# Kernel tuning notes

Measured on AMD Instinct MI355X. Metric: run time of the kernel, lower is better.

The kernel has to match this reference:

```python
import jax, jax.numpy as jnp
import numpy as np

N_LAYERS = 5
HID = 64
N_FF = 512
N_VOCAB = 500
N_NODES = 50000
N_EDGES = 800000


def setup_inputs() -> dict:
    key = jax.random.key(0)
    ks = jax.random.split(key, 12)
    x = jax.random.randint(ks[0], (N_NODES,), 0, N_VOCAB)
    edge_index = jax.random.randint(ks[1], (2, N_EDGES), 0, N_NODES)
    edge_attr = jax.random.normal(ks[2], (N_EDGES, 4), dtype=jnp.float32)
    s = 1.0 / float(np.sqrt(HID))
    vert_emb = jax.random.normal(ks[3], (N_VOCAB + 1, HID), dtype=jnp.float32) * s
    vert_emb = vert_emb.at[N_VOCAB].set(0.0)  # padding_idx row
    edge_emb_w = jax.random.normal(ks[4], (4, HID), dtype=jnp.float32) * 0.5
    edge_lin_w = jax.random.normal(ks[5], (N_LAYERS, HID, HID), dtype=jnp.float32) * s
    rel_w = jax.random.normal(ks[6], (N_LAYERS, HID, HID), dtype=jnp.float32) * s
    rel_b = jnp.zeros((N_LAYERS, HID), dtype=jnp.float32)
    root_w = jax.random.normal(ks[7], (N_LAYERS, HID, HID), dtype=jnp.float32) * s
    res_w = jax.random.normal(ks[8], (N_LAYERS, HID, HID), dtype=jnp.float32) * s
    head_w1 = jax.random.normal(ks[9], (HID, N_FF), dtype=jnp.float32) * s
    head_b1 = jnp.zeros((N_FF,), dtype=jnp.float32)
    head_w2 = jax.random.normal(ks[10], (N_FF, 1), dtype=jnp.float32) * (1.0 / float(np.sqrt(N_FF)))
    head_b2 = jnp.zeros((1,), dtype=jnp.float32)
    return dict(x=x, edge_index=edge_index, edge_attr=edge_attr, vert_emb=vert_emb,
                edge_emb_w=edge_emb_w, edge_lin_w=edge_lin_w, rel_w=rel_w, rel_b=rel_b,
                root_w=root_w, res_w=res_w, head_w1=head_w1, head_b1=head_b1,
                head_w2=head_w2, head_b2=head_b2)


def reference(x, edge_index, edge_attr, vert_emb, edge_emb_w, edge_lin_w, rel_w, rel_b,
              root_w, res_w, head_w1, head_b1, head_w2, head_b2):
    src, dst = edge_index[0], edge_index[1]
    h = vert_emb[x]                         # [N, HID] embedding lookup
    ea = edge_attr @ edge_emb_w             # [E, HID] edge embedding
    n = h.shape[0]
    for l in range(N_LAYERS):
        ea_l = ea @ edge_lin_w[l]           # ResGraphModule.edge_lin
        # GraphConv(aggr='add'): lin_rel(scatter_add(x_src * e)) + lin_root(x)
        msg = h[src] * ea_l                 # [E, HID] gather + modulate
        agg = jax.ops.segment_sum(msg, dst, num_segments=n)
        out = agg @ rel_w[l] + rel_b[l] + h @ root_w[l]
        out = jax.nn.relu(out)
        h = out + h @ res_w[l]              # residual branch (res_lin)
    # head MLP (dropout is identity in eval mode); torch GELU is exact erf GELU
    hft = jax.nn.gelu(h @ head_w1 + head_b1, approximate=False)
    return hft @ head_w2 + head_b2          # [N, 1]
```

## Files before the change

kernel.cpp:

```cpp
#include <hip/hip_runtime.h>
#include <math.h>

#define HID 64
#define NLAY 5
#define NFF 512

typedef __attribute__((ext_vector_type(8))) short bf16x8;
typedef __attribute__((ext_vector_type(4))) float f32x4;

__device__ __forceinline__ unsigned short f2bf(float x) {
  unsigned int b = __float_as_uint(x);
  b += 0x7FFFu + ((b >> 16) & 1u);
  return (unsigned short)(b >> 16);
}
__device__ __forceinline__ float bf2f(unsigned short u) {
  return __uint_as_float((unsigned int)u << 16);
}

__global__ void prep_wl_kernel(const float* __restrict__ edge_emb_w,
                               const float* __restrict__ edge_lin_w,
                               float* __restrict__ Wl) {
  int l = blockIdx.x;
  int t = threadIdx.x;
  int j = t >> 6;
  int d = t & 63;
  const float* ew = edge_emb_w + j * HID;
  const float* lw = edge_lin_w + l * HID * HID;
  float acc = 0.f;
#pragma unroll
  for (int k = 0; k < HID; ++k) acc = fmaf(ew[k], lw[k * HID + d], acc);
  Wl[(l * 4 + j) * HID + d] = acc;
}

__global__ void prep_w1b_kernel(const float* __restrict__ w1,
                                unsigned short* __restrict__ w1bhi,
                                unsigned short* __restrict__ w1blo) {
  int t = blockIdx.x * 256 + threadIdx.x;
  int f = t >> 6;
  int l = t & 63;
  int kt = f >> 5;
  int nt = f & 31;
  int krow = kt * 32 + (l >> 4) * 8;
  int col = nt * 16 + (l & 15);
#pragma unroll
  for (int j = 0; j < 8; ++j) {
    float v = w1[(size_t)(krow + j) * NFF + col];
    unsigned short hi = f2bf(v);
    unsigned short lo = f2bf(v - bf2f(hi));
    w1bhi[(size_t)t * 8 + j] = hi;
    w1blo[(size_t)t * 8 + j] = lo;
  }
}

__global__ void prep_nw_kernel(const float* __restrict__ rel_w,
                               const float* __restrict__ root_w,
                               const float* __restrict__ res_w,
                               unsigned short* __restrict__ nwhi,
                               unsigned short* __restrict__ nwlo) {
  int mi = blockIdx.x;
  int layer = mi / 3, mat = mi % 3;
  const float* W = (mat == 0 ? rel_w : (mat == 1 ? root_w : res_w)) +
                   (size_t)layer * HID * HID;
  int t = threadIdx.x;
  int f = t >> 6, l = t & 63;
  int kt = f >> 2, nt = f & 3;
  int krow = kt * 32 + (l >> 4) * 8;
  int col = nt * 16 + (l & 15);
#pragma unroll
  for (int j = 0; j < 8; ++j) {
    float v = W[(size_t)(krow + j) * HID + col];
    unsigned short hi = f2bf(v);
    unsigned short lo = f2bf(v - bf2f(hi));
    size_t off = (((size_t)mi * 8 + f) * 64 + l) * 8 + j;
    nwhi[off] = hi;
    nwlo[off] = lo;
  }
}

__global__ void embed_kernel(const int* __restrict__ x,
                             const float* __restrict__ vert_emb,
                             float* __restrict__ h,
                             unsigned short* __restrict__ h16, int n) {
  int idx = blockIdx.x * blockDim.x + threadIdx.x;
  if (idx >= n * HID) return;
  int node = idx >> 6;
  int d = idx & 63;
  float v = vert_emb[x[node] * HID + d];
  h[idx] = v;
  h16[idx] = f2bf(v);
}


__global__ void zero_deg_kernel(int* __restrict__ deg, int n) {
  int i = blockIdx.x * blockDim.x + threadIdx.x;
  if (i < n) deg[i] = 0;
}

__global__ void hist_kernel(const int* __restrict__ dst, int* __restrict__ deg, int E) {
  int e = blockIdx.x * blockDim.x + threadIdx.x;
  if (e < E) atomicAdd(&deg[dst[e]], 1);
}

__global__ void bsum_kernel(const int* __restrict__ deg, int* __restrict__ bsum, int n) {
  __shared__ int s[256];
  int t = threadIdx.x;
  int i = blockIdx.x * 256 + t;
  s[t] = (i < n) ? deg[i] : 0;
  __syncthreads();
#pragma unroll
  for (int off = 128; off > 0; off >>= 1) {
    if (t < off) s[t] += s[t + off];
    __syncthreads();
  }
  if (t == 0) bsum[blockIdx.x] = s[0];
}

__global__ void bscan_kernel(const int* __restrict__ bsum, int* __restrict__ boff, int nb) {
  __shared__ int s[256];
  int t = threadIdx.x;
  int v = (t < nb) ? bsum[t] : 0;
  s[t] = v;
  __syncthreads();
#pragma unroll
  for (int off = 1; off < 256; off <<= 1) {
    int u = (t >= off) ? s[t - off] : 0;
    __syncthreads();
    s[t] += u;
    __syncthreads();
  }
  if (t < nb) boff[t] = s[t] - v;
}

__global__ void scan3_kernel(const int* __restrict__ deg, const int* __restrict__ boff,
                             int* __restrict__ row_ptr, int* __restrict__ cursor, int n) {
  __shared__ int s[256];
  int t = threadIdx.x;
  int i = blockIdx.x * 256 + t;
  int v = (i < n) ? deg[i] : 0;
  s[t] = v;
  __syncthreads();
#pragma unroll
  for (int off = 1; off < 256; off <<= 1) {
    int u = (t >= off) ? s[t - off] : 0;
    __syncthreads();
    s[t] += u;
    __syncthreads();
  }
  if (i < n) {
    int excl = boff[blockIdx.x] + s[t] - v;
    row_ptr[i] = excl;
    cursor[i] = excl;
    if (i == n - 1) row_ptr[n] = excl + v;
  }
}

__global__ void scatter_kernel(const int* __restrict__ src,
                               const int* __restrict__ dst,
                               const float4* __restrict__ edge_attr,
                               int* __restrict__ cursor,
                               float4* __restrict__ csr2, int E) {
  int e = blockIdx.x * blockDim.x + threadIdx.x;
  if (e >= E) return;
  int pos = atomicAdd(&cursor[dst[e]], 1);
  csr2[(size_t)2 * pos] = edge_attr[e];
  float4 m;
  m.x = __int_as_float(src[e]);
  m.y = 0.f; m.z = 0.f; m.w = 0.f;
  csr2[(size_t)2 * pos + 1] = m;
}

__global__ __launch_bounds__(256, 8)
void gather_kernel(const int* __restrict__ row_ptr,
                   const float4* __restrict__ csr2,
                   const float* __restrict__ Wl,
                   const unsigned short* __restrict__ h16,
                   float* __restrict__ agg, int n) {
  int wid = threadIdx.x >> 6;
  int d = threadIdx.x & 63;
  int node = blockIdx.x * 4 + wid;
  if (node >= n) return;
  int beg = __builtin_amdgcn_readfirstlane(row_ptr[node]);
  int end = __builtin_amdgcn_readfirstlane(row_ptr[node + 1]);
  const int* csri = (const int*)csr2;
  float P0 = 0.f, P1 = 0.f, P2 = 0.f, P3 = 0.f;
  int j = beg;
  for (; j + 16 <= end; j += 16) {
    int ss[16];
    float hh[16];
    float4 ee[16];
#pragma unroll
    for (int u = 0; u < 16; ++u) ss[u] = csri[((size_t)2 * (j + u) + 1) * 4];
#pragma unroll
    for (int u = 0; u < 16; ++u) hh[u] = bf2f(h16[(size_t)ss[u] * HID + d]);
#pragma unroll
    for (int u = 0; u < 16; ++u) ee[u] = csr2[(size_t)2 * (j + u)];
#pragma unroll
    for (int u = 0; u < 16; ++u) {
      P0 = fmaf(ee[u].x, hh[u], P0);
      P1 = fmaf(ee[u].y, hh[u], P1);
      P2 = fmaf(ee[u].z, hh[u], P2);
      P3 = fmaf(ee[u].w, hh[u], P3);
    }
  }
  for (; j + 4 <= end; j += 4) {
    int ss[4];
    float hh[4];
    float4 ee[4];
#pragma unroll
    for (int u = 0; u < 4; ++u) ss[u] = csri[((size_t)2 * (j + u) + 1) * 4];
#pragma unroll
    for (int u = 0; u < 4; ++u) hh[u] = bf2f(h16[(size_t)ss[u] * HID + d]);
#pragma unroll
    for (int u = 0; u < 4; ++u) ee[u] = csr2[(size_t)2 * (j + u)];
#pragma unroll
    for (int u = 0; u < 4; ++u) {
      P0 = fmaf(ee[u].x, hh[u], P0);
      P1 = fmaf(ee[u].y, hh[u], P1);
      P2 = fmaf(ee[u].z, hh[u], P2);
      P3 = fmaf(ee[u].w, hh[u], P3);
    }
  }
  for (; j < end; ++j) {
    int s0 = csri[((size_t)2 * j + 1) * 4];
    float4 e0 = csr2[(size_t)2 * j];
    float h0 = bf2f(h16[(size_t)s0 * HID + d]);
    P0 = fmaf(e0.x, h0, P0);
    P1 = fmaf(e0.y, h0, P1);
    P2 = fmaf(e0.z, h0, P2);
    P3 = fmaf(e0.w, h0, P3);
  }
  float acc = P0 * Wl[d];
  acc = fmaf(P1, Wl[HID + d], acc);
  acc = fmaf(P2, Wl[2 * HID + d], acc);
  acc = fmaf(P3, Wl[3 * HID + d], acc);
  agg[(size_t)node * HID + d] = acc;
}

__global__ __launch_bounds__(256, 4)
void node_mfma_kernel(const float* __restrict__ h,
                      const unsigned short* __restrict__ h16,
                      const float* __restrict__ agg,
                      const unsigned short* __restrict__ nwhi,
                      const unsigned short* __restrict__ nwlo,
                      const float* __restrict__ rel_b,
                      float* __restrict__ hn,
                      unsigned short* __restrict__ hn16, int n) {
  int tid = threadIdx.x;
  int w = tid >> 6;
  int l = tid & 63;
  int q = l & 15;
  int g = l >> 4;
  int base = blockIdx.x * 16;
  int node = base + q;
  if (node >= n) node = n - 1;
  bf16x8 aghi[2], aglo[2], ahhi[2], ahlo[2];
#pragma unroll
  for (int kt = 0; kt < 2; ++kt) {
    int koff = kt * 32 + g * 8;
    const float* ap = agg + (size_t)node * HID + koff;
    const float* hp = h + (size_t)node * HID + koff;
    ahhi[kt] = *(const bf16x8*)(h16 + (size_t)node * HID + koff);
#pragma unroll
    for (int j = 0; j < 8; ++j) {
      float av = ap[j];
      unsigned short hi = f2bf(av);
      aghi[kt][j] = (short)hi;
      aglo[kt][j] = (short)f2bf(av - bf2f(hi));
      float r = hp[j] - bf2f((unsigned short)ahhi[kt][j]);
      ahlo[kt][j] = (short)f2bf(r);
    }
  }
  f32x4 aR = {0.f, 0.f, 0.f, 0.f};
  f32x4 aO = {0.f, 0.f, 0.f, 0.f};
  f32x4 aS = {0.f, 0.f, 0.f, 0.f};
#pragma unroll
  for (int kt = 0; kt < 2; ++kt) {
    int f = kt * 4 + w;
    const bf16x8* bRh = (const bf16x8*)(nwhi + (((size_t)0 * 8 + f) * 64 + l) * 8);
    const bf16x8* bRl = (const bf16x8*)(nwlo + (((size_t)0 * 8 + f) * 64 + l) * 8);
    const bf16x8* bOh = (const bf16x8*)(nwhi + (((size_t)1 * 8 + f) * 64 + l) * 8);
    const bf16x8* bOl = (const bf16x8*)(nwlo + (((size_t)1 * 8 + f) * 64 + l) * 8);
    const bf16x8* bSh = (const bf16x8*)(nwhi + (((size_t)2 * 8 + f) * 64 + l) * 8);
    const bf16x8* bSl = (const bf16x8*)(nwlo + (((size_t)2 * 8 + f) * 64 + l) * 8);
    aR = __builtin_amdgcn_mfma_f32_16x16x32_bf16(aglo[kt], *bRh, aR, 0, 0, 0);
    aR = __builtin_amdgcn_mfma_f32_16x16x32_bf16(aghi[kt], *bRl, aR, 0, 0, 0);
    aR = __builtin_amdgcn_mfma_f32_16x16x32_bf16(aghi[kt], *bRh, aR, 0, 0, 0);
    aO = __builtin_amdgcn_mfma_f32_16x16x32_bf16(ahlo[kt], *bOh, aO, 0, 0, 0);
    aO = __builtin_amdgcn_mfma_f32_16x16x32_bf16(ahhi[kt], *bOl, aO, 0, 0, 0);
    aO = __builtin_amdgcn_mfma_f32_16x16x32_bf16(ahhi[kt], *bOh, aO, 0, 0, 0);
    aS = __builtin_amdgcn_mfma_f32_16x16x32_bf16(ahlo[kt], *bSh, aS, 0, 0, 0);
    aS = __builtin_amdgcn_mfma_f32_16x16x32_bf16(ahhi[kt], *bSl, aS, 0, 0, 0);
    aS = __builtin_amdgcn_mfma_f32_16x16x32_bf16(ahhi[kt], *bSh, aS, 0, 0, 0);
  }
  int col = w * 16 + q;
  float bd = rel_b[col];
#pragma unroll
  for (int r = 0; r < 4; ++r) {
    int nd = base + g * 4 + r;
    if (nd < n) {
      float v = fmaxf(aR[r] + aO[r] + bd, 0.f) + aS[r];
      hn[(size_t)nd * HID + col] = v;
      hn16[(size_t)nd * HID + col] = f2bf(v);
    }
  }
}

__global__ __launch_bounds__(256, 4)
void head_kernel(const float* __restrict__ h,
                 const unsigned short* __restrict__ h16,
                 const unsigned short* __restrict__ w1bhi,
                 const unsigned short* __restrict__ w1blo,
                 const float* __restrict__ b1,
                 const float* __restrict__ w2,
                 const float* __restrict__ b2,
                 float* __restrict__ out, int n) {
  __shared__ float red[4][16];
  int tid = threadIdx.x;
  int w = tid >> 6;
  int l = tid & 63;
  int row = l & 15;
  int g = l >> 4;
  int base = blockIdx.x * 16;
  int node = base + row;
  if (node >= n) node = n - 1;
  f32x4 acc[8];
#pragma unroll
  for (int t = 0; t < 8; ++t) acc[t] = (f32x4){0.f, 0.f, 0.f, 0.f};
#pragma unroll
  for (int kt = 0; kt < 2; ++kt) {
    int koff = kt * 32 + g * 8;
    bf16x8 ahi = *(const bf16x8*)(h16 + (size_t)node * HID + koff);
    const float* hp = h + (size_t)node * HID + koff;
    bf16x8 alo;
#pragma unroll
    for (int j = 0; j < 8; ++j) {
      float r = hp[j] - bf2f((unsigned short)ahi[j]);
      alo[j] = (short)f2bf(r);
    }
#pragma unroll
    for (int t = 0; t < 8; ++t) {
      int f = kt * 32 + w * 8 + t;
      bf16x8 bhi = *(const bf16x8*)(w1bhi + (size_t)f * 512 + l * 8);
      bf16x8 blo = *(const bf16x8*)(w1blo + (size_t)f * 512 + l * 8);
      acc[t] = __builtin_amdgcn_mfma_f32_16x16x32_bf16(alo, bhi, acc[t], 0, 0, 0);
      acc[t] = __builtin_amdgcn_mfma_f32_16x16x32_bf16(ahi, blo, acc[t], 0, 0, 0);
      acc[t] = __builtin_amdgcn_mfma_f32_16x16x32_bf16(ahi, bhi, acc[t], 0, 0, 0);
    }
  }
  float s0 = 0.f, s1 = 0.f, s2 = 0.f, s3 = 0.f;
#pragma unroll
  for (int t = 0; t < 8; ++t) {
    int ff = (w * 8 + t) * 16 + row;
    float bb = b1[ff];
    float ww = w2[ff];
    float xv, gl;
    xv = acc[t][0] + bb; gl = 0.5f * xv * (1.f + erff(xv * 0.70710678118654752f)); s0 = fmaf(gl, ww, s0);
    xv = acc[t][1] + bb; gl = 0.5f * xv * (1.f + erff(xv * 0.70710678118654752f)); s1 = fmaf(gl, ww, s1);
    xv = acc[t][2] + bb; gl = 0.5f * xv * (1.f + erff(xv * 0.70710678118654752f)); s2 = fmaf(gl, ww, s2);
    xv = acc[t][3] + bb; gl = 0.5f * xv * (1.f + erff(xv * 0.70710678118654752f)); s3 = fmaf(gl, ww, s3);
  }
#pragma unroll
  for (int off = 1; off < 16; off <<= 1) {
    s0 += __shfl_xor(s0, off);
    s1 += __shfl_xor(s1, off);
    s2 += __shfl_xor(s2, off);
    s3 += __shfl_xor(s3, off);
  }
  if ((l & 15) == 0) {
    red[w][g * 4 + 0] = s0;
    red[w][g * 4 + 1] = s1;
    red[w][g * 4 + 2] = s2;
    red[w][g * 4 + 3] = s3;
  }
  __syncthreads();
  if (tid < 16 && base + tid < n)
    out[base + tid] = red[0][tid] + red[1][tid] + red[2][tid] + red[3][tid] + b2[0];
}

extern "C" void kernel_launch(void* const* d_in, const int* in_sizes, int n_in,
                              void* d_out, int out_size, void* d_ws, size_t ws_size,
                              hipStream_t stream) {
  const int*   x          = (const int*)d_in[0];
  const int*   edge_index = (const int*)d_in[1];
  const float* edge_attr  = (const float*)d_in[2];
  const float* vert_emb   = (const float*)d_in[3];
  const float* edge_emb_w = (const float*)d_in[4];
  const float* edge_lin_w = (const float*)d_in[5];
  const float* rel_w      = (const float*)d_in[6];
  const float* rel_b      = (const float*)d_in[7];
  const float* root_w     = (const float*)d_in[8];
  const float* res_w      = (const float*)d_in[9];
  const float* w1         = (const float*)d_in[10];
  const float* b1         = (const float*)d_in[11];
  const float* w2         = (const float*)d_in[12];
  const float* b2         = (const float*)d_in[13];

  const int n = in_sizes[0];
  const int E = in_sizes[2] / 4;
  const int* src = edge_index;
  const int* dst = edge_index + E;
  const int nb = (n + 255) / 256;

  float* ws   = (float*)d_ws;
  float* Wl   = ws;
  float* hA   = ws + 2048;
  float* hB   = hA + (size_t)n * HID;
  float* agg  = hB + (size_t)n * HID;
  float4* csr2 = (float4*)(agg + (size_t)n * HID);
  int* row_ptr = (int*)(csr2 + (size_t)2 * E);
  int* cursor  = row_ptr + (n + 1);
  int* deg     = cursor + n;
  int* bsum    = deg + n;
  int* boff    = bsum + 256;
  unsigned short* w1bhi = (unsigned short*)(((size_t)(boff + 256) + 15) & ~(size_t)15);
  unsigned short* w1blo = w1bhi + 64 * 512;
  unsigned short* nwhi  = w1blo + 64 * 512;
  unsigned short* nwlo  = nwhi + NLAY * 3 * 4096;
  unsigned short* h16A  = nwlo + NLAY * 3 * 4096;
  unsigned short* h16B  = h16A + (size_t)n * HID;

  prep_wl_kernel<<<dim3(NLAY), dim3(256), 0, stream>>>(edge_emb_w, edge_lin_w, Wl);
  prep_w1b_kernel<<<dim3(16), dim3(256), 0, stream>>>(w1, w1bhi, w1blo);
  prep_nw_kernel<<<dim3(NLAY * 3), dim3(512), 0, stream>>>(rel_w, root_w, res_w, nwhi, nwlo);

  int totalHD = n * HID;
  embed_kernel<<<dim3((totalHD + 255) / 256), dim3(256), 0, stream>>>(
      x, vert_emb, hA, h16A, n);

  zero_deg_kernel<<<dim3((n + 255) / 256), dim3(256), 0, stream>>>(deg, n);
  hist_kernel<<<dim3((E + 255) / 256), dim3(256), 0, stream>>>(dst, deg, E);
  bsum_kernel<<<dim3(nb), dim3(256), 0, stream>>>(deg, bsum, n);
  bscan_kernel<<<dim3(1), dim3(256), 0, stream>>>(bsum, boff, nb);
  scan3_kernel<<<dim3(nb), dim3(256), 0, stream>>>(deg, boff, row_ptr, cursor, n);
  scatter_kernel<<<dim3((E + 255) / 256), dim3(256), 0, stream>>>(
      src, dst, (const float4*)edge_attr, cursor, csr2, E);

  float* hc = hA;
  float* hx = hB;
  unsigned short* h16c = h16A;
  unsigned short* h16x = h16B;
  for (int l = 0; l < NLAY; ++l) {
    gather_kernel<<<dim3((n + 3) / 4), dim3(256), 0, stream>>>(
        row_ptr, csr2, Wl + l * 4 * HID, h16c, agg, n);
    node_mfma_kernel<<<dim3((n + 15) / 16), dim3(256), 0, stream>>>(
        hc, h16c, agg, nwhi + (size_t)l * 3 * 4096, nwlo + (size_t)l * 3 * 4096,
        rel_b + l * HID, hx, h16x, n);
    float* t = hc; hc = hx; hx = t;
    unsigned short* t16 = h16c; h16c = h16x; h16x = t16;
  }

  head_kernel<<<dim3((n + 15) / 16), dim3(256), 0, stream>>>(
      hc, h16c, w1bhi, w1blo, b1, w2, b2, (float*)d_out, n);
}
```

Baseline: 453.7 us.

## Fuse per-layer gather into node MFMA kernel via shared-memory aggregation

Merges the per-layer edge gather and the node MFMA update into one kernel. Each block gathers aggregates for its 16 nodes into shared memory, then runs the MFMA stage, so the global agg buffer round trip and one launch per layer are removed. The three weight-prep kernels are also merged into one, and deg zeroing moves into the embed kernel. The cost is that each wave now handles 4 nodes serially under launch_bounds(256,4) instead of (256,8), which lowers occupancy and latency hiding for the irregular gather.

Result: no change. 451.3 us (-0.5%).

```diff
diff --git a/kernel.cpp b/kernel.cpp
--- a/kernel.cpp
+++ b/kernel.cpp
@@ -17,70 +17,74 @@
   return __uint_as_float((unsigned int)u << 16);
 }
 
-__global__ void prep_wl_kernel(const float* __restrict__ edge_emb_w,
-                               const float* __restrict__ edge_lin_w,
-                               float* __restrict__ Wl) {
-  int l = blockIdx.x;
-  int t = threadIdx.x;
-  int j = t >> 6;
-  int d = t & 63;
-  const float* ew = edge_emb_w + j * HID;
-  const float* lw = edge_lin_w + l * HID * HID;
-  float acc = 0.f;
-#pragma unroll
-  for (int k = 0; k < HID; ++k) acc = fmaf(ew[k], lw[k * HID + d], acc);
-  Wl[(l * 4 + j) * HID + d] = acc;
-}
-
-__global__ void prep_w1b_kernel(const float* __restrict__ w1,
+__global__ void prep_all_kernel(const float* __restrict__ edge_emb_w,
+                                const float* __restrict__ edge_lin_w,
+                                const float* __restrict__ w1,
+                                const float* __restrict__ rel_w,
+                                const float* __restrict__ root_w,
+                                const float* __restrict__ res_w,
+                                float* __restrict__ Wl,
                                 unsigned short* __restrict__ w1bhi,
-                                unsigned short* __restrict__ w1blo) {
-  int t = blockIdx.x * 256 + threadIdx.x;
-  int f = t >> 6;
-  int l = t & 63;
-  int kt = f >> 5;
-  int nt = f & 31;
-  int krow = kt * 32 + (l >> 4) * 8;
-  int col = nt * 16 + (l & 15);
-#pragma unroll
-  for (int j = 0; j < 8; ++j) {
-    float v = w1[(size_t)(krow + j) * NFF + col];
-    unsigned short hi = f2bf(v);
-    unsigned short lo = f2bf(v - bf2f(hi));
-    w1bhi[(size_t)t * 8 + j] = hi;
-    w1blo[(size_t)t * 8 + j] = lo;
-  }
-}
-
-__global__ void prep_nw_kernel(const float* __restrict__ rel_w,
-                               const float* __restrict__ root_w,
-                               const float* __restrict__ res_w,
-                               unsigned short* __restrict__ nwhi,
-                               unsigned short* __restrict__ nwlo) {
-  int mi = blockIdx.x;
-  int layer = mi / 3, mat = mi % 3;
-  const float* W = (mat == 0 ? rel_w : (mat == 1 ? root_w : res_w)) +
-                   (size_t)layer * HID * HID;
-  int t = threadIdx.x;
-  int f = t >> 6, l = t & 63;
-  int kt = f >> 2, nt = f & 3;
-  int krow = kt * 32 + (l >> 4) * 8;
-  int col = nt * 16 + (l & 15);
-#pragma unroll
-  for (int j = 0; j < 8; ++j) {
-    float v = W[(size_t)(krow + j) * HID + col];
-    unsigned short hi = f2bf(v);
-    unsigned short lo = f2bf(v - bf2f(hi));
-    size_t off = (((size_t)mi * 8 + f) * 64 + l) * 8 + j;
-    nwhi[off] = hi;
-    nwlo[off] = lo;
+                                unsigned short* __restrict__ w1blo,
+                                unsigned short* __restrict__ nwhi,
+                                unsigned short* __restrict__ nwlo) {
+  int bid = blockIdx.x;
+  int tid = threadIdx.x;
+  if (bid < 5) {
+    int j = tid >> 6;
+    int d = tid & 63;
+    const float* ew = edge_emb_w + j * HID;
+    const float* lw = edge_lin_w + bid * HID * HID;
+    float acc = 0.f;
+#pragma unroll
+    for (int k = 0; k < HID; ++k) acc = fmaf(ew[k], lw[k * HID + d], acc);
+    Wl[(bid * 4 + j) * HID + d] = acc;
+  } else if (bid < 21) {
+    int t = (bid - 5) * 256 + tid;
+    int f = t >> 6;
+    int l = t & 63;
+    int kt = f >> 5;
+    int nt = f & 31;
+    int krow = kt * 32 + (l >> 4) * 8;
+    int col = nt * 16 + (l & 15);
+#pragma unroll
+    for (int j = 0; j < 8; ++j) {
+      float v = w1[(size_t)(krow + j) * NFF + col];
+      unsigned short hi = f2bf(v);
+      unsigned short lo = f2bf(v - bf2f(hi));
+      w1bhi[(size_t)t * 8 + j] = hi;
+      w1blo[(size_t)t * 8 + j] = lo;
+    }
+  } else {
+    int mi = bid - 21;
+    int layer = mi / 3, mat = mi % 3;
+    const float* W = (mat == 0 ? rel_w : (mat == 1 ? root_w : res_w)) +
+                     (size_t)layer * HID * HID;
+#pragma unroll
+    for (int half = 0; half < 2; ++half) {
+      int t = half * 256 + tid;
+      int f = t >> 6, l = t & 63;
+      int kt = f >> 2, nt = f & 3;
+      int krow = kt * 32 + (l >> 4) * 8;
+      int col = nt * 16 + (l & 15);
+#pragma unroll
+      for (int j = 0; j < 8; ++j) {
+        float v = W[(size_t)(krow + j) * HID + col];
+        unsigned short hi = f2bf(v);
+        unsigned short lo = f2bf(v - bf2f(hi));
+        size_t off = (((size_t)mi * 8 + f) * 64 + l) * 8 + j;
+        nwhi[off] = hi;
+        nwlo[off] = lo;
+      }
+    }
   }
 }
 
 __global__ void embed_kernel(const int* __restrict__ x,
                              const float* __restrict__ vert_emb,
                              float* __restrict__ h,
-                             unsigned short* __restrict__ h16, int n) {
+                             unsigned short* __restrict__ h16,
+                             int* __restrict__ deg, int n) {
   int idx = blockIdx.x * blockDim.x + threadIdx.x;
   if (idx >= n * HID) return;
   int node = idx >> 6;
@@ -88,13 +92,9 @@
   float v = vert_emb[x[node] * HID + d];
   h[idx] = v;
   h16[idx] = f2bf(v);
-}
-
-
-__global__ void zero_deg_kernel(int* __restrict__ deg, int n) {
-  int i = blockIdx.x * blockDim.x + threadIdx.x;
-  if (i < n) deg[i] = 0;
-}
+  if (d == 0) deg[node] = 0;
+}
+
 
 __global__ void hist_kernel(const int* __restrict__ dst, int* __restrict__ deg, int E) {
   int e = blockIdx.x * blockDim.x + threadIdx.x;
@@ -169,100 +169,95 @@
   csr2[(size_t)2 * pos + 1] = m;
 }
 
-__global__ __launch_bounds__(256, 8)
-void gather_kernel(const int* __restrict__ row_ptr,
-                   const float4* __restrict__ csr2,
-                   const float* __restrict__ Wl,
-                   const unsigned short* __restrict__ h16,
-                   float* __restrict__ agg, int n) {
-  int wid = threadIdx.x >> 6;
-  int d = threadIdx.x & 63;
-  int node = blockIdx.x * 4 + wid;
-  if (node >= n) return;
-  int beg = __builtin_amdgcn_readfirstlane(row_ptr[node]);
-  int end = __builtin_amdgcn_readfirstlane(row_ptr[node + 1]);
-  const int* csri = (const int*)csr2;
-  float P0 = 0.f, P1 = 0.f, P2 = 0.f, P3 = 0.f;
-  int j = beg;
-  for (; j + 16 <= end; j += 16) {
-    int ss[16];
-    float hh[16];
-    float4 ee[16];
-#pragma unroll
-    for (int u = 0; u < 16; ++u) ss[u] = csri[((size_t)2 * (j + u) + 1) * 4];
-#pragma unroll
-    for (int u = 0; u < 16; ++u) hh[u] = bf2f(h16[(size_t)ss[u] * HID + d]);
-#pragma unroll
-    for (int u = 0; u < 16; ++u) ee[u] = csr2[(size_t)2 * (j + u)];
-#pragma unroll
-    for (int u = 0; u < 16; ++u) {
-      P0 = fmaf(ee[u].x, hh[u], P0);
-      P1 = fmaf(ee[u].y, hh[u], P1);
-      P2 = fmaf(ee[u].z, hh[u], P2);
-      P3 = fmaf(ee[u].w, hh[u], P3);
-    }
-  }
-  for (; j + 4 <= end; j += 4) {
-    int ss[4];
-    float hh[4];
-    float4 ee[4];
-#pragma unroll
-    for (int u = 0; u < 4; ++u) ss[u] = csri[((size_t)2 * (j + u) + 1) * 4];
-#pragma unroll
-    for (int u = 0; u < 4; ++u) hh[u] = bf2f(h16[(size_t)ss[u] * HID + d]);
-#pragma unroll
-    for (int u = 0; u < 4; ++u) ee[u] = csr2[(size_t)2 * (j + u)];
-#pragma unroll
-    for (int u = 0; u < 4; ++u) {
-      P0 = fmaf(ee[u].x, hh[u], P0);
-      P1 = fmaf(ee[u].y, hh[u], P1);
-      P2 = fmaf(ee[u].z, hh[u], P2);
-      P3 = fmaf(ee[u].w, hh[u], P3);
-    }
-  }
-  for (; j < end; ++j) {
-    int s0 = csri[((size_t)2 * j + 1) * 4];
-    float4 e0 = csr2[(size_t)2 * j];
-    float h0 = bf2f(h16[(size_t)s0 * HID + d]);
-    P0 = fmaf(e0.x, h0, P0);
-    P1 = fmaf(e0.y, h0, P1);
-    P2 = fmaf(e0.z, h0, P2);
-    P3 = fmaf(e0.w, h0, P3);
-  }
-  float acc = P0 * Wl[d];
-  acc = fmaf(P1, Wl[HID + d], acc);
-  acc = fmaf(P2, Wl[2 * HID + d], acc);
-  acc = fmaf(P3, Wl[3 * HID + d], acc);
-  agg[(size_t)node * HID + d] = acc;
-}
-
 __global__ __launch_bounds__(256, 4)
-void node_mfma_kernel(const float* __restrict__ h,
-                      const unsigned short* __restrict__ h16,
-                      const float* __restrict__ agg,
-                      const unsigned short* __restrict__ nwhi,
-                      const unsigned short* __restrict__ nwlo,
-                      const float* __restrict__ rel_b,
-                      float* __restrict__ hn,
-                      unsigned short* __restrict__ hn16, int n) {
+void layer_fused_kernel(const int* __restrict__ row_ptr,
+                        const float4* __restrict__ csr2,
+                        const float* __restrict__ Wl,
+                        const float* __restrict__ h,
+                        const unsigned short* __restrict__ h16,
+                        const unsigned short* __restrict__ nwhi,
+                        const unsigned short* __restrict__ nwlo,
+                        const float* __restrict__ rel_b,
+                        float* __restrict__ hn,
+                        unsigned short* __restrict__ hn16, int n) {
+  __shared__ float sagg[16][65];
   int tid = threadIdx.x;
   int w = tid >> 6;
+  int d = tid & 63;
+  int base = blockIdx.x * 16;
+  float w0 = Wl[d], w1_ = Wl[HID + d], w2_ = Wl[2 * HID + d], w3_ = Wl[3 * HID + d];
+  const int* csri = (const int*)csr2;
+  for (int i = 0; i < 4; ++i) {
+    int node = base + w * 4 + i;
+    float P0 = 0.f, P1 = 0.f, P2 = 0.f, P3 = 0.f;
+    if (node < n) {
+      int beg = __builtin_amdgcn_readfirstlane(row_ptr[node]);
+      int end = __builtin_amdgcn_readfirstlane(row_ptr[node + 1]);
+      int j = beg;
+      for (; j + 16 <= end; j += 16) {
+        int ss[16];
+        float hh[16];
+        float4 ee[16];
+#pragma unroll
+        for (int u = 0; u < 16; ++u) ss[u] = csri[((size_t)2 * (j + u) + 1) * 4];
+#pragma unroll
+        for (int u = 0; u < 16; ++u) hh[u] = bf2f(h16[(size_t)ss[u] * HID + d]);
+#pragma unroll
+        for (int u = 0; u < 16; ++u) ee[u] = csr2[(size_t)2 * (j + u)];
+#pragma unroll
+        for (int u = 0; u < 16; ++u) {
+          P0 = fmaf(ee[u].x, hh[u], P0);
+          P1 = fmaf(ee[u].y, hh[u], P1);
+          P2 = fmaf(ee[u].z, hh[u], P2);
+          P3 = fmaf(ee[u].w, hh[u], P3);
+        }
+      }
+      for (; j + 4 <= end; j += 4) {
+        int ss[4];
+        float hh[4];
+        float4 ee[4];
+#pragma unroll
+        for (int u = 0; u < 4; ++u) ss[u] = csri[((size_t)2 * (j + u) + 1) * 4];
+#pragma unroll
+        for (int u = 0; u < 4; ++u) hh[u] = bf2f(h16[(size_t)ss[u] * HID + d]);
+#pragma unroll
+        for (int u = 0; u < 4; ++u) ee[u] = csr2[(size_t)2 * (j + u)];
+#pragma unroll
+        for (int u = 0; u < 4; ++u) {
+          P0 = fmaf(ee[u].x, hh[u], P0);
+          P1 = fmaf(ee[u].y, hh[u], P1);
+          P2 = fmaf(ee[u].z, hh[u], P2);
+          P3 = fmaf(ee[u].w, hh[u], P3);
+        }
+      }
+      for (; j < end; ++j) {
+        int s0 = csri[((size_t)2 * j + 1) * 4];
+        float4 e0 = csr2[(size_t)2 * j];
+        float h0 = bf2f(h16[(size_t)s0 * HID + d]);
+        P0 = fmaf(e0.x, h0, P0);
+        P1 = fmaf(e0.y, h0, P1);
+        P2 = fmaf(e0.z, h0, P2);
+        P3 = fmaf(e0.w, h0, P3);
+      }
+    }
+    float acc = fmaf(P3, w3_, fmaf(P2, w2_, fmaf(P1, w1_, P0 * w0)));
+    sagg[w * 4 + i][d] = acc;
+  }
+  __syncthreads();
   int l = tid & 63;
   int q = l & 15;
   int g = l >> 4;
-  int base = blockIdx.x * 16;
   int node = base + q;
   if (node >= n) node = n - 1;
   bf16x8 aghi[2], aglo[2], ahhi[2], ahlo[2];
 #pragma unroll
   for (int kt = 0; kt < 2; ++kt) {
     int koff = kt * 32 + g * 8;
-    const float* ap = agg + (size_t)node * HID + koff;
     const float* hp = h + (size_t)node * HID + koff;
     ahhi[kt] = *(const bf16x8*)(h16 + (size_t)node * HID + koff);
 #pragma unroll
     for (int j = 0; j < 8; ++j) {
-      float av = ap[j];
+      float av = sagg[q][koff + j];
       unsigned short hi = f2bf(av);
       aghi[kt][j] = (short)hi;
       aglo[kt][j] = (short)f2bf(av - bf2f(hi));
@@ -405,8 +400,7 @@
   float* Wl   = ws;
   float* hA   = ws + 2048;
   float* hB   = hA + (size_t)n * HID;
-  float* agg  = hB + (size_t)n * HID;
-  float4* csr2 = (float4*)(agg + (size_t)n * HID);
+  float4* csr2 = (float4*)(hB + (size_t)n * HID);
   int* row_ptr = (int*)(csr2 + (size_t)2 * E);
   int* cursor  = row_ptr + (n + 1);
   int* deg     = cursor + n;
@@ -419,15 +413,14 @@
   unsigned short* h16A  = nwlo + NLAY * 3 * 4096;
   unsigned short* h16B  = h16A + (size_t)n * HID;
 
-  prep_wl_kernel<<<dim3(NLAY), dim3(256), 0, stream>>>(edge_emb_w, edge_lin_w, Wl);
-  prep_w1b_kernel<<<dim3(16), dim3(256), 0, stream>>>(w1, w1bhi, w1blo);
-  prep_nw_kernel<<<dim3(NLAY * 3), dim3(512), 0, stream>>>(rel_w, root_w, res_w, nwhi, nwlo);
+  prep_all_kernel<<<dim3(36), dim3(256), 0, stream>>>(
+      edge_emb_w, edge_lin_w, w1, rel_w, root_w, res_w,
+      Wl, w1bhi, w1blo, nwhi, nwlo);
 
   int totalHD = n * HID;
   embed_kernel<<<dim3((totalHD + 255) / 256), dim3(256), 0, stream>>>(
-      x, vert_emb, hA, h16A, n);
-
-  zero_deg_kernel<<<dim3((n + 255) / 256), dim3(256), 0, stream>>>(deg, n);
+      x, vert_emb, hA, h16A, deg, n);
+
   hist_kernel<<<dim3((E + 255) / 256), dim3(256), 0, stream>>>(dst, deg, E);
   bsum_kernel<<<dim3(nb), dim3(256), 0, stream>>>(deg, bsum, n);
   bscan_kernel<<<dim3(1), dim3(256), 0, stream>>>(bsum, boff, nb);
@@ -440,10 +433,9 @@
   unsigned short* h16c = h16A;
   unsigned short* h16x = h16B;
   for (int l = 0; l < NLAY; ++l) {
-    gather_kernel<<<dim3((n + 3) / 4), dim3(256), 0, stream>>>(
-        row_ptr, csr2, Wl + l * 4 * HID, h16c, agg, n);
-    node_mfma_kernel<<<dim3((n + 15) / 16), dim3(256), 0, stream>>>(
-        hc, h16c, agg, nwhi + (size_t)l * 3 * 4096, nwlo + (size_t)l * 3 * 4096,
+    layer_fused_kernel<<<dim3((n + 15) / 16), dim3(256), 0, stream>>>(
+        row_ptr, csr2, Wl + l * 4 * HID, hc, h16c,
+        nwhi + (size_t)l * 3 * 4096, nwlo + (size_t)l * 3 * 4096,
         rel_b + l * HID, hx, h16x, n);
     float* t = hc; hc = hx; hx = t;
     unsigned short* t16 = h16c; h16c = h16x; h16x = t16;
```
